# Performance work log

Measured on AMD Instinct MI355X. Metric: run time of the kernel, lower is better.

Reference implementation:

```python
import jax, jax.numpy as jnp
import numpy as np

G, N, K, F = 256, 512, 6, 64  # graphs, nodes/graph, knn k, n_features
T = G * N

def leaky(x):
    return jnp.where(x >= 0, x, 0.2 * x)

def prelu(x, a):
    return jnp.where(x >= 0, x, a * x)

def knn_idx(x):
    # per-graph kNN (k=6, self excluded); idx[i] = global indices of 6 nearest nbrs of i
    xg = x.reshape(G, N, F)
    sq = jnp.sum(xg * xg, axis=-1)                       # [G,N]
    d = sq[:, :, None] + sq[:, None, :] - 2.0 * jnp.einsum('gnf,gmf->gnm', xg, xg)
    d = jnp.where(jnp.eye(N, dtype=bool)[None], jnp.inf, d)  # loop=False
    _, idx = jax.lax.top_k(-d, K)                        # [G,N,K] local indices
    idx = idx + (jnp.arange(G) * N)[:, None, None]       # make global
    return idx.reshape(T, K)

def gconv(h, idx, W, b):
    # PyG GeneralConv defaults: out[i] = sum_{j in nbr(i)} (x_j W + b) + x_i
    s = jnp.take(h, idx, axis=0).sum(axis=1)             # [T,F] sum of neighbor feats
    return s @ W + K * b + h

def forward(x, W1, b1, a1, W2, b2, a2,
            Wc1, bc1, Wc2, bc2, Wc3, bc3, Wc4, bc4,
            W3, b3, a3, W4, b4, a4,
            Wh1, bh1, Wh2, bh2, Wh3, bh3, Wh4, bh4, idx):
    h = prelu(x @ W1 + b1, a1)
    h = prelu(h @ W2 + b2, a2)
    h = gconv(h, idx, Wc1, bc1)
    h = gconv(h, idx, Wc2, bc2)
    h = gconv(h, idx, Wc3, bc3)
    h = gconv(h, idx, Wc4, bc4)
    h = prelu(h @ W3 + b3, a3)
    h = prelu(h @ W4 + b4, a4)
    pooled = h.reshape(G, N, F).sum(axis=1)              # global_add_pool -> [G,F]
    y = leaky(pooled @ Wh1 + bh1)
    y = leaky(y @ Wh2 + bh2)
    y = leaky(y @ Wh3 + bh3)
    return y @ Wh4 + bh4                                 # [G,1]

def setup_inputs():
    key = jax.random.key(0)
    ks = jax.random.split(key, 16)
    def lin(k, i, o):
        k1, k2 = jax.random.split(k)
        s = 1.0 / np.sqrt(i)
        return (jax.random.uniform(k1, (i, o), jnp.float32, -s, s),
                jax.random.uniform(k2, (o,), jnp.float32, -s, s))
    inp = {"x": jax.random.normal(ks[0], (T, F), jnp.float32)}
    W1, b1 = lin(ks[1], F, F); W2, b2 = lin(ks[2], F, F)
    Wc1, bc1 = lin(ks[3], F, F); Wc2, bc2 = lin(ks[4], F, F)
    Wc3, bc3 = lin(ks[5], F, F); Wc4, bc4 = lin(ks[6], F, F)
    W3, b3 = lin(ks[7], F, F); W4, b4 = lin(ks[8], F, F)
    Wh1, bh1 = lin(ks[9], F, 4 * F); Wh2, bh2 = lin(ks[10], 4 * F, 4 * F)
    Wh3, bh3 = lin(ks[11], 4 * F, F); Wh4, bh4 = lin(ks[12], F, 1)
    a = 0.25 * jnp.ones((F,), jnp.float32)  # PReLU init
    inp.update(W1=W1, b1=b1, a1=a, W2=W2, b2=b2, a2=a,
               Wc1=Wc1, bc1=bc1, Wc2=Wc2, bc2=bc2, Wc3=Wc3, bc3=bc3, Wc4=Wc4, bc4=bc4,
               W3=W3, b3=b3, a3=a, W4=W4, b4=b4, a4=a,
               Wh1=Wh1, bh1=bh1, Wh2=Wh2, bh2=bh2, Wh3=Wh3, bh3=bh3, Wh4=Wh4, bh4=bh4)
    return inp

def reference(x, W1, b1, a1, W2, b2, a2, Wc1, bc1, Wc2, bc2, Wc3, bc3, Wc4, bc4,
              W3, b3, a3, W4, b4, a4, Wh1, bh1, Wh2, bh2, Wh3, bh3, Wh4, bh4):
    idx = knn_idx(x)  # edge_index built from raw x, as in the torch module
    return forward(x, W1, b1, a1, W2, b2, a2, Wc1, bc1, Wc2, bc2, Wc3, bc3, Wc4, bc4,
                   W3, b3, a3, W4, b4, a4, Wh1, bh1, Wh2, bh2, Wh3, bh3, Wh4, bh4, idx)
```

## Files before the change

kernel.cpp:

```cpp
#include <hip/hip_runtime.h>

#define NGRAPH 256
#define NNODE  512
#define KNN    6
#define NCAND  12
#define NF     64
#define SBF    72
#define NT     768
#define NW     12
#define PBF    18432
#define CANDO  PBF
#define SQO    (PBF + 3072)
#define WTO    36864
#define LDS_FLOATS 39168
#define LDS_BYTES  (LDS_FLOATS*4)
#define POOLP  PBF
#define POOLED (PBF + 1024)
#define Y1OFF  (PBF + 1088)
#define Y2OFF  (PBF + 1344)
#define Y3OFF  (PBF + 1600)
#define BIG 1e30f

typedef float v4f __attribute__((ext_vector_type(4)));
typedef float v2f __attribute__((ext_vector_type(2)));
typedef short v8s __attribute__((ext_vector_type(8)));

struct Params {
  const float *x;
  const float *W1,*b1,*a1, *W2,*b2,*a2;
  const float *Wc0,*bc0, *Wc1,*bc1, *Wc2,*bc2, *Wc3,*bc3;
  const float *W3,*b3,*a3, *W4,*b4,*a4;
  const float *Wh1,*bh1, *Wh2,*bh2, *Wh3,*bh3, *Wh4,*bh4;
  float *out;
};

__device__ __forceinline__ unsigned f2bf(float x) {
  union { float f; unsigned u; } cc; cc.f = x;
  unsigned u = cc.u;
  return (u + 0x7FFFu + ((u >> 16) & 1u)) >> 16;
}
__device__ __forceinline__ float bflo(unsigned u) {
  union { unsigned u; float f; } c; c.u = u << 16; return c.f;
}
__device__ __forceinline__ float bfhi(unsigned u) {
  union { unsigned u; float f; } c; c.u = u & 0xffff0000u; return c.f;
}
__device__ __forceinline__ v2f up2(unsigned u) {
  v2f r; r.x = bflo(u); r.y = bfhi(u); return r;
}

__device__ __forceinline__ v8s bfrag(const unsigned short* base, int row, int c0) {
  return *(const v8s*)(base + row*SBF + c0);
}

__device__ __forceinline__ float packe(float e, int j) {
  return __uint_as_float((__float_as_uint(e) & 0xFFFFFE00u) | (unsigned)j);
}

__device__ __forceinline__ void ins8(float (&b)[8], float v) {
  if (v < b[7]) {
#pragma unroll
    for (int p = 0; p < 8; ++p) {
      float lo = fminf(b[p], v);
      v = fmaxf(b[p], v);
      b[p] = lo;
    }
  }
}
__device__ __forceinline__ void ins12(float (&b)[NCAND], float v) {
  if (v < b[NCAND-1]) {
#pragma unroll
    for (int p = 0; p < NCAND; ++p) {
      float lo = fminf(b[p], v);
      v = fmaxf(b[p], v);
      b[p] = lo;
    }
  }
}

__device__ __forceinline__ void stage_wt(const float* W, unsigned short* wt, int tid) {
  const int col = tid >> 3, ks = (tid & 7) * 8;
  const float* wp = W + col;
  unsigned d[4];
#pragma unroll
  for (int i = 0; i < 4; ++i) {
    unsigned lo = f2bf(wp[(ks + 2*i    ) * NF]);
    unsigned hi = f2bf(wp[(ks + 2*i + 1) * NF]);
    d[i] = lo | (hi << 16);
  }
  *(uint4*)&wt[col*SBF + ks] = make_uint4(d[0], d[1], d[2], d[3]);
}

__global__ __launch_bounds__(NT) void fused_gnn(Params P) {
  extern __shared__ float lds[];
  unsigned short* hbf  = (unsigned short*)lds;
  unsigned short* pbf  = (unsigned short*)&lds[PBF];
  unsigned short* wt   = (unsigned short*)&lds[WTO];
  unsigned short* cand = (unsigned short*)&lds[CANDO];
  const int tid  = threadIdx.x;
  const int g    = blockIdx.x;
  const int rA   = tid;
  const int lane = tid & 63;
  const int w    = tid >> 6;
  const int c    = lane & 15;
  const int qq   = lane >> 4;

  const float* xgp = P.x + (size_t)g * NNODE * NF;
  const float4* xg = (const float4*)xgp;

#pragma unroll 1
  for (int i = tid; i < NNODE*NF/4; i += NT) {
    float4 v = xg[i];
    int row = i >> 4, k4 = i & 15;
    unsigned lo = f2bf(v.x) | (f2bf(v.y) << 16);
    unsigned hi = f2bf(v.z) | (f2bf(v.w) << 16);
    *(uint2*)&hbf[row*SBF + 4*k4] = make_uint2(lo, hi);
  }
  __syncthreads();

  if (tid < 512) {
    const uint4* xr = (const uint4*)(hbf + rA*SBF);
    float s = 0.f;
#pragma unroll
    for (int k = 0; k < 8; ++k) {
      uint4 u = xr[k];
      float f;
      f = bflo(u.x); s = fmaf(f, f, s); f = bfhi(u.x); s = fmaf(f, f, s);
      f = bflo(u.y); s = fmaf(f, f, s); f = bfhi(u.y); s = fmaf(f, f, s);
      f = bflo(u.z); s = fmaf(f, f, s); f = bfhi(u.z); s = fmaf(f, f, s);
      f = bflo(u.w); s = fmaf(f, f, s); f = bfhi(u.w); s = fmaf(f, f, s);
    }
    lds[SQO + rA] = s;
  }
  __syncthreads();

  {
#pragma unroll 1
    for (int tt = w; tt < 32; tt += NW) {
      const int i0 = tt * 16;
      v8s A0 = bfrag(hbf, i0 + c, qq*8);
      v8s A1 = bfrag(hbf, i0 + c, 32 + qq*8);
      const int myrow = i0 + c;

      float d8[8];
#pragma unroll
      for (int m = 0; m < 8; ++m) d8[m] = BIG;

#pragma unroll 2
      for (int jt = 0; jt < 32; ++jt) {
        const int j0 = jt * 16;
        v8s B0 = bfrag(hbf, j0 + c, qq*8);
        v8s B1 = bfrag(hbf, j0 + c, 32 + qq*8);
        v4f acc = {0.f, 0.f, 0.f, 0.f};
        acc = __builtin_amdgcn_mfma_f32_16x16x32_bf16(B0, A0, acc, 0, 0, 0);
        acc = __builtin_amdgcn_mfma_f32_16x16x32_bf16(B1, A1, acc, 0, 0, 0);
        float4 sv = *(const float4*)&lds[SQO + j0 + qq*4];
        float e0 = fmaf(-2.f, acc[0], sv.x);
        float e1 = fmaf(-2.f, acc[1], sv.y);
        float e2 = fmaf(-2.f, acc[2], sv.z);
        float e3 = fmaf(-2.f, acc[3], sv.w);
        const int jb = j0 + qq*4;
        if (jt == tt) {
          if (jb     == myrow) e0 = BIG;
          if (jb + 1 == myrow) e1 = BIG;
          if (jb + 2 == myrow) e2 = BIG;
          if (jb + 3 == myrow) e3 = BIG;
        }
        ins8(d8, packe(e0, jb));
        ins8(d8, packe(e1, jb+1));
        ins8(d8, packe(e2, jb+2));
        ins8(d8, packe(e3, jb+3));
      }

      float cd[NCAND];
#pragma unroll
      for (int m = 0; m < 8; ++m) cd[m] = d8[m];
#pragma unroll
      for (int m = 8; m < NCAND; ++m) cd[m] = BIG;
      {
        float pd[8];
#pragma unroll
        for (int s = 0; s < 8; ++s) pd[s] = __shfl_xor(cd[s], 16);
#pragma unroll
        for (int s = 0; s < 8; ++s) ins12(cd, pd[s]);
      }
      {
        float pd[NCAND];
#pragma unroll
        for (int s = 0; s < NCAND; ++s) pd[s] = __shfl_xor(cd[s], 32);
#pragma unroll
        for (int s = 0; s < NCAND; ++s) ins12(cd, pd[s]);
      }
      if (lane < 16) {
#pragma unroll
        for (int s = 0; s < NCAND; ++s)
          cand[(i0 + lane)*NCAND + s] =
            (unsigned short)(__float_as_uint(cd[s]) & 0x1FFu);
      }
    }
  }
  __syncthreads();

  if (tid < 512) {
    const float4* xrow = (const float4*)(xgp + rA*NF);
    float s0 = 0.f;
#pragma unroll
    for (int k4 = 0; k4 < 16; ++k4) {
      float4 a = xrow[k4];
      s0 = fmaf(a.x,a.x,s0); s0 = fmaf(a.y,a.y,s0); s0 = fmaf(a.z,a.z,s0); s0 = fmaf(a.w,a.w,s0);
    }
    lds[SQO + rA] = s0;
  }
  __syncthreads();

  int nbrA[KNN];
  if (tid < 512) {
    const float4* xrow = (const float4*)(xgp + rA*NF);
    float nd[6]; int ni[6];
#pragma unroll
    for (int m = 0; m < 6; ++m) { nd[m] = BIG; ni[m] = 0x7fffffff; }
    int cnd[NCAND];
#pragma unroll
    for (int s = 0; s < NCAND; ++s) cnd[s] = cand[rA*NCAND + s];

#pragma unroll 1
    for (int s = 0; s < NCAND; ++s) {
      int j = cnd[s];
      const float4* xj = (const float4*)(xgp + j*NF);
      float4 aa = {0.f, 0.f, 0.f, 0.f};
#pragma unroll
      for (int k4 = 0; k4 < 16; ++k4) {
        float4 a = xrow[k4];
        float4 v = xj[k4];
        aa.x = fmaf(a.x, v.x, aa.x); aa.y = fmaf(a.y, v.y, aa.y);
        aa.z = fmaf(a.z, v.z, aa.z); aa.w = fmaf(a.w, v.w, aa.w);
      }
      float e = fmaf(-2.f, (aa.x+aa.y)+(aa.z+aa.w), lds[SQO + j]);
      if (e < nd[5] || (e == nd[5] && j < ni[5])) {
#pragma unroll
        for (int pp = 0; pp < 6; ++pp) {
          bool lt = (e < nd[pp]) || (e == nd[pp] && j < ni[pp]);
          float tb2 = nd[pp]; int ti = ni[pp];
          nd[pp] = lt ? e : tb2;  ni[pp] = lt ? j : ti;
          e      = lt ? tb2 : e;  j      = lt ? ti : j;
        }
      }
    }
#pragma unroll
    for (int m = 0; m < 6; ++m) nbrA[m] = ni[m];
  }

#pragma unroll 1
  for (int L = 0; L < 8; ++L) {
    const bool isconv = (L >= 2 && L <= 5);
    const float* Wl = L==0?P.W1 : L==1?P.W2 : L==2?P.Wc0 : L==3?P.Wc1 :
                      L==4?P.Wc2 : L==5?P.Wc3 : L==6?P.W3 : P.W4;
    const float* bl = L==0?P.b1 : L==1?P.b2 : L==2?P.bc0 : L==3?P.bc1 :
                      L==4?P.bc2 : L==5?P.bc3 : L==6?P.b3 : P.b4;
    const float* al = L==0?P.a1 : L==1?P.a2 : L==6?P.a3 : P.a4;

    __syncthreads();
    if (tid < 512) stage_wt(Wl, wt, tid);
    __syncthreads();

    v8s B0[4], B1[4];
#pragma unroll
    for (int n = 0; n < 4; ++n) {
      B0[n] = bfrag(wt, n*16 + c, qq*8);
      B1[n] = bfrag(wt, n*16 + c, 32 + qq*8);
    }
    float br[4], ar[4];
    if (!isconv) {
#pragma unroll
      for (int n = 0; n < 4; ++n) { br[n] = bl[n*16 + c]; ar[n] = al[n*16 + c]; }
    }

#pragma unroll 1
    for (int tt = w; tt < 32; tt += NW) {
      const int i0 = tt * 16;
      v8s A0 = bfrag(hbf, i0 + c, qq*8);
      v8s A1 = bfrag(hbf, i0 + c, 32 + qq*8);
#pragma unroll
      for (int n = 0; n < 4; ++n) {
        v4f acc = {0.f, 0.f, 0.f, 0.f};
        acc = __builtin_amdgcn_mfma_f32_16x16x32_bf16(A0, B0[n], acc, 0, 0, 0);
        acc = __builtin_amdgcn_mfma_f32_16x16x32_bf16(A1, B1[n], acc, 0, 0, 0);
        if (isconv) {
#pragma unroll
          for (int r = 0; r < 4; ++r)
            pbf[(i0 + qq*4 + r)*SBF + n*16 + c] = (unsigned short)f2bf(acc[r]);
        } else {
#pragma unroll
          for (int r = 0; r < 4; ++r) {
            float v = acc[r] + br[n];
            v = v >= 0.f ? v : ar[n]*v;
            hbf[(i0 + qq*4 + r)*SBF + n*16 + c] = (unsigned short)f2bf(v);
          }
        }
      }
    }

    if (isconv) {
      __syncthreads();
      if (tid < 512) {
        const float4* bp = (const float4*)bl;
#pragma unroll 1
        for (int ch = 0; ch < 4; ++ch) {
          const int co = ch*16;
          v2f a2[8];
          {
            const uint4* hr = (const uint4*)&hbf[rA*SBF + co];
            uint4 u0 = hr[0], u1 = hr[1];
            a2[0]=up2(u0.x); a2[1]=up2(u0.y); a2[2]=up2(u0.z); a2[3]=up2(u0.w);
            a2[4]=up2(u1.x); a2[5]=up2(u1.y); a2[6]=up2(u1.z); a2[7]=up2(u1.w);
          }
          {
            float4 b0 = bp[ch*4+0], b1 = bp[ch*4+1], b2 = bp[ch*4+2], b3 = bp[ch*4+3];
            v2f t;
            t.x=b0.x; t.y=b0.y; a2[0] += 6.f*t;  t.x=b0.z; t.y=b0.w; a2[1] += 6.f*t;
            t.x=b1.x; t.y=b1.y; a2[2] += 6.f*t;  t.x=b1.z; t.y=b1.w; a2[3] += 6.f*t;
            t.x=b2.x; t.y=b2.y; a2[4] += 6.f*t;  t.x=b2.z; t.y=b2.w; a2[5] += 6.f*t;
            t.x=b3.x; t.y=b3.y; a2[6] += 6.f*t;  t.x=b3.z; t.y=b3.w; a2[7] += 6.f*t;
          }
#pragma unroll
          for (int mm = 0; mm < KNN; ++mm) {
            const uint4* pr = (const uint4*)&pbf[nbrA[mm]*SBF + co];
            uint4 p0 = pr[0], p1 = pr[1];
            a2[0]+=up2(p0.x); a2[1]+=up2(p0.y); a2[2]+=up2(p0.z); a2[3]+=up2(p0.w);
            a2[4]+=up2(p1.x); a2[5]+=up2(p1.y); a2[6]+=up2(p1.z); a2[7]+=up2(p1.w);
          }
          uint4 o0, o1;
          o0.x = f2bf(a2[0].x) | (f2bf(a2[0].y) << 16);
          o0.y = f2bf(a2[1].x) | (f2bf(a2[1].y) << 16);
          o0.z = f2bf(a2[2].x) | (f2bf(a2[2].y) << 16);
          o0.w = f2bf(a2[3].x) | (f2bf(a2[3].y) << 16);
          o1.x = f2bf(a2[4].x) | (f2bf(a2[4].y) << 16);
          o1.y = f2bf(a2[5].x) | (f2bf(a2[5].y) << 16);
          o1.z = f2bf(a2[6].x) | (f2bf(a2[6].y) << 16);
          o1.w = f2bf(a2[7].x) | (f2bf(a2[7].y) << 16);
          uint4* hw = (uint4*)&hbf[rA*SBF + co];
          hw[0] = o0; hw[1] = o1;
        }
      }
    }
  }
  __syncthreads();

  if (tid < 512) {
    int f2 = tid & 31, cch = tid >> 5;
    int rstart = cch * 32;
    const unsigned* h32 = (const unsigned*)hbf;
    v2f s2; s2.x = 0.f; s2.y = 0.f;
#pragma unroll 1
    for (int r = 0; r < 32; ++r) s2 += up2(h32[(rstart + r)*(SBF/2) + f2]);
    *(float2*)&lds[POOLP + cch*64 + 2*f2] = make_float2(s2.x, s2.y);
  }
  __syncthreads();
  if (tid < 64) {
    float pool = 0.f;
#pragma unroll
    for (int cc = 0; cc < 16; ++cc) pool += lds[POOLP + cc*64 + tid];
    lds[POOLED + tid] = pool;
  }
  __syncthreads();

  if (tid < 256) {
    float acc = P.bh1[tid];
#pragma unroll 4
    for (int k = 0; k < 64; ++k) acc = fmaf(lds[POOLED+k], P.Wh1[k*256 + tid], acc);
    lds[Y1OFF + tid] = acc >= 0.f ? acc : 0.2f*acc;
  }
  __syncthreads();
  if (tid < 512) {
    int o = tid & 255, hh = tid >> 8;
    float acc = hh ? 0.f : P.bh2[o];
    const int k0 = hh * 128;
#pragma unroll 4
    for (int k = k0; k < k0 + 128; ++k) acc = fmaf(lds[Y1OFF+k], P.Wh2[k*256 + o], acc);
    lds[POOLP + hh*256 + o] = acc;
  }
  __syncthreads();
  if (tid < 256) {
    float acc = lds[POOLP + tid] + lds[POOLP + 256 + tid];
    lds[Y2OFF + tid] = acc >= 0.f ? acc : 0.2f*acc;
  }
  __syncthreads();
  if (tid < 64) {
    float acc = P.bh3[tid];
#pragma unroll 4
    for (int k = 0; k < 256; ++k) acc = fmaf(lds[Y2OFF+k], P.Wh3[k*64 + tid], acc);
    lds[Y3OFF + tid] = acc >= 0.f ? acc : 0.2f*acc;
  }
  __syncthreads();
  if (tid == 0) {
    float acc = P.bh4[0];
#pragma unroll 4
    for (int k = 0; k < 64; ++k) acc = fmaf(lds[Y3OFF+k], P.Wh4[k], acc);
    P.out[g] = acc;
  }
}

extern "C" void kernel_launch(void* const* d_in, const int* in_sizes, int n_in,
                              void* d_out, int out_size, void* d_ws, size_t ws_size,
                              hipStream_t stream) {
  Params P;
  P.x   = (const float*)d_in[0];
  P.W1  = (const float*)d_in[1];  P.b1  = (const float*)d_in[2];  P.a1 = (const float*)d_in[3];
  P.W2  = (const float*)d_in[4];  P.b2  = (const float*)d_in[5];  P.a2 = (const float*)d_in[6];
  P.Wc0 = (const float*)d_in[7];  P.bc0 = (const float*)d_in[8];
  P.Wc1 = (const float*)d_in[9];  P.bc1 = (const float*)d_in[10];
  P.Wc2 = (const float*)d_in[11]; P.bc2 = (const float*)d_in[12];
  P.Wc3 = (const float*)d_in[13]; P.bc3 = (const float*)d_in[14];
  P.W3  = (const float*)d_in[15]; P.b3  = (const float*)d_in[16]; P.a3 = (const float*)d_in[17];
  P.W4  = (const float*)d_in[18]; P.b4  = (const float*)d_in[19]; P.a4 = (const float*)d_in[20];
  P.Wh1 = (const float*)d_in[21]; P.bh1 = (const float*)d_in[22];
  P.Wh2 = (const float*)d_in[23]; P.bh2 = (const float*)d_in[24];
  P.Wh3 = (const float*)d_in[25]; P.bh3 = (const float*)d_in[26];
  P.Wh4 = (const float*)d_in[27]; P.bh4 = (const float*)d_in[28];
  P.out = (float*)d_out;

  (void)hipFuncSetAttribute(reinterpret_cast<const void*>(fused_gnn),
                            hipFuncAttributeMaxDynamicSharedMemorySize, LDS_BYTES);

  fused_gnn<<<NGRAPH, NT, LDS_BYTES, stream>>>(P);
}
```

Before: 314.6 us.

## Rebalance kNN filter tiles per wave, spread gconv gather over all threads, parallelize head tail

The kNN MFMA filter previously gave 12 waves a strided set of the 32 row tiles, which left the work uneven. Now waves 0-7 take 3 tiles each and waves 8-11 take 2, and each wave shares every B-fragment load across its tiles. Neighbor indices move from per-thread registers to LDS, so the gconv aggregation can run on all 768 threads with 8 lanes per row covering 8 features each, instead of 512 threads looping over 4 chunks. The last two head layers are also split across 256 threads, with a wave shuffle reduction for the final dot product. The costs are more registers in the multi-tile filter and extra LDS space and traffic for the neighbor table.

```diff
diff --git a/kernel.cpp b/kernel.cpp
--- a/kernel.cpp
+++ b/kernel.cpp
@@ -12,13 +12,13 @@
 #define CANDO  PBF
 #define SQO    (PBF + 3072)
 #define WTO    36864
-#define LDS_FLOATS 39168
+#define NBRO   39168
+#define LDS_FLOATS 40704
 #define LDS_BYTES  (LDS_FLOATS*4)
 #define POOLP  PBF
 #define POOLED (PBF + 1024)
 #define Y1OFF  (PBF + 1088)
 #define Y2OFF  (PBF + 1344)
-#define Y3OFF  (PBF + 1600)
 #define BIG 1e30f
 
 typedef float v4f __attribute__((ext_vector_type(4)));
@@ -91,12 +91,89 @@
   *(uint4*)&wt[col*SBF + ks] = make_uint4(d[0], d[1], d[2], d[3]);
 }
 
+template<int NTILE>
+__device__ __forceinline__ void filter_tiles(const unsigned short* hbf,
+                                             const float* ldsf,
+                                             unsigned short* cand,
+                                             const int (&tts)[NTILE],
+                                             int lane, int c, int qq) {
+  v8s A0[NTILE], A1[NTILE];
+  float d8[NTILE][8];
+  int i0[NTILE];
+#pragma unroll
+  for (int k = 0; k < NTILE; ++k) {
+    i0[k] = tts[k] * 16;
+    A0[k] = bfrag(hbf, i0[k] + c, qq*8);
+    A1[k] = bfrag(hbf, i0[k] + c, 32 + qq*8);
+#pragma unroll
+    for (int m = 0; m < 8; ++m) d8[k][m] = BIG;
+  }
+#pragma unroll 1
+  for (int jt = 0; jt < 32; ++jt) {
+    const int j0 = jt * 16;
+    v8s B0 = bfrag(hbf, j0 + c, qq*8);
+    v8s B1 = bfrag(hbf, j0 + c, 32 + qq*8);
+    float4 sv = *(const float4*)&ldsf[SQO + j0 + qq*4];
+    const int jb = j0 + qq*4;
+#pragma unroll
+    for (int k = 0; k < NTILE; ++k) {
+      v4f acc = {0.f, 0.f, 0.f, 0.f};
+      acc = __builtin_amdgcn_mfma_f32_16x16x32_bf16(B0, A0[k], acc, 0, 0, 0);
+      acc = __builtin_amdgcn_mfma_f32_16x16x32_bf16(B1, A1[k], acc, 0, 0, 0);
+      float e0 = fmaf(-2.f, acc[0], sv.x);
+      float e1 = fmaf(-2.f, acc[1], sv.y);
+      float e2 = fmaf(-2.f, acc[2], sv.z);
+      float e3 = fmaf(-2.f, acc[3], sv.w);
+      if (jt == tts[k]) {
+        const int myrow = i0[k] + c;
+        if (jb     == myrow) e0 = BIG;
+        if (jb + 1 == myrow) e1 = BIG;
+        if (jb + 2 == myrow) e2 = BIG;
+        if (jb + 3 == myrow) e3 = BIG;
+      }
+      ins8(d8[k], packe(e0, jb));
+      ins8(d8[k], packe(e1, jb+1));
+      ins8(d8[k], packe(e2, jb+2));
+      ins8(d8[k], packe(e3, jb+3));
+    }
+  }
+#pragma unroll
+  for (int k = 0; k < NTILE; ++k) {
+    float cd[NCAND];
+#pragma unroll
+    for (int m = 0; m < 8; ++m) cd[m] = d8[k][m];
+#pragma unroll
+    for (int m = 8; m < NCAND; ++m) cd[m] = BIG;
+    {
+      float pd[8];
+#pragma unroll
+      for (int s = 0; s < 8; ++s) pd[s] = __shfl_xor(cd[s], 16);
+#pragma unroll
+      for (int s = 0; s < 8; ++s) ins12(cd, pd[s]);
+    }
+    {
+      float pd[NCAND];
+#pragma unroll
+      for (int s = 0; s < NCAND; ++s) pd[s] = __shfl_xor(cd[s], 32);
+#pragma unroll
+      for (int s = 0; s < NCAND; ++s) ins12(cd, pd[s]);
+    }
+    if (lane < 16) {
+#pragma unroll
+      for (int s = 0; s < NCAND; ++s)
+        cand[(i0[k] + lane)*NCAND + s] =
+          (unsigned short)(__float_as_uint(cd[s]) & 0x1FFu);
+    }
+  }
+}
+
 __global__ __launch_bounds__(NT) void fused_gnn(Params P) {
   extern __shared__ float lds[];
   unsigned short* hbf  = (unsigned short*)lds;
   unsigned short* pbf  = (unsigned short*)&lds[PBF];
   unsigned short* wt   = (unsigned short*)&lds[WTO];
   unsigned short* cand = (unsigned short*)&lds[CANDO];
+  unsigned short* nbrs = (unsigned short*)&lds[NBRO];
   const int tid  = threadIdx.x;
   const int g    = blockIdx.x;
   const int rA   = tid;
@@ -134,70 +211,12 @@
   }
   __syncthreads();
 
-  {
-#pragma unroll 1
-    for (int tt = w; tt < 32; tt += NW) {
-      const int i0 = tt * 16;
-      v8s A0 = bfrag(hbf, i0 + c, qq*8);
-      v8s A1 = bfrag(hbf, i0 + c, 32 + qq*8);
-      const int myrow = i0 + c;
-
-      float d8[8];
-#pragma unroll
-      for (int m = 0; m < 8; ++m) d8[m] = BIG;
-
-#pragma unroll 2
-      for (int jt = 0; jt < 32; ++jt) {
-        const int j0 = jt * 16;
-        v8s B0 = bfrag(hbf, j0 + c, qq*8);
-        v8s B1 = bfrag(hbf, j0 + c, 32 + qq*8);
-        v4f acc = {0.f, 0.f, 0.f, 0.f};
-        acc = __builtin_amdgcn_mfma_f32_16x16x32_bf16(B0, A0, acc, 0, 0, 0);
-        acc = __builtin_amdgcn_mfma_f32_16x16x32_bf16(B1, A1, acc, 0, 0, 0);
-        float4 sv = *(const float4*)&lds[SQO + j0 + qq*4];
-        float e0 = fmaf(-2.f, acc[0], sv.x);
-        float e1 = fmaf(-2.f, acc[1], sv.y);
-        float e2 = fmaf(-2.f, acc[2], sv.z);
-        float e3 = fmaf(-2.f, acc[3], sv.w);
-        const int jb = j0 + qq*4;
-        if (jt == tt) {
-          if (jb     == myrow) e0 = BIG;
-          if (jb + 1 == myrow) e1 = BIG;
-          if (jb + 2 == myrow) e2 = BIG;
-          if (jb + 3 == myrow) e3 = BIG;
-        }
-        ins8(d8, packe(e0, jb));
-        ins8(d8, packe(e1, jb+1));
-        ins8(d8, packe(e2, jb+2));
-        ins8(d8, packe(e3, jb+3));
-      }
-
-      float cd[NCAND];
-#pragma unroll
-      for (int m = 0; m < 8; ++m) cd[m] = d8[m];
-#pragma unroll
-      for (int m = 8; m < NCAND; ++m) cd[m] = BIG;
-      {
-        float pd[8];
-#pragma unroll
-        for (int s = 0; s < 8; ++s) pd[s] = __shfl_xor(cd[s], 16);
-#pragma unroll
-        for (int s = 0; s < 8; ++s) ins12(cd, pd[s]);
-      }
-      {
-        float pd[NCAND];
-#pragma unroll
-        for (int s = 0; s < NCAND; ++s) pd[s] = __shfl_xor(cd[s], 32);
-#pragma unroll
-        for (int s = 0; s < NCAND; ++s) ins12(cd, pd[s]);
-      }
-      if (lane < 16) {
-#pragma unroll
-        for (int s = 0; s < NCAND; ++s)
-          cand[(i0 + lane)*NCAND + s] =
-            (unsigned short)(__float_as_uint(cd[s]) & 0x1FFu);
-      }
-    }
+  if (w < 8) {
+    int tts[3] = {w, w + 8, w + 16};
+    filter_tiles<3>(hbf, lds, cand, tts, lane, c, qq);
+  } else {
+    int tts[2] = {w + 16, w + 20};
+    filter_tiles<2>(hbf, lds, cand, tts, lane, c, qq);
   }
   __syncthreads();
 
@@ -213,7 +232,6 @@
   }
   __syncthreads();
 
-  int nbrA[KNN];
   if (tid < 512) {
     const float4* xrow = (const float4*)(xgp + rA*NF);
     float nd[6]; int ni[6];
@@ -247,7 +265,7 @@
       }
     }
 #pragma unroll
-    for (int m = 0; m < 6; ++m) nbrA[m] = ni[m];
+    for (int m = 0; m < 6; ++m) nbrs[rA*KNN + m] = (unsigned short)ni[m];
   }
 
 #pragma unroll 1
@@ -302,44 +320,33 @@
 
     if (isconv) {
       __syncthreads();
-      if (tid < 512) {
-        const float4* bp = (const float4*)bl;
-#pragma unroll 1
-        for (int ch = 0; ch < 4; ++ch) {
-          const int co = ch*16;
-          v2f a2[8];
-          {
-            const uint4* hr = (const uint4*)&hbf[rA*SBF + co];
-            uint4 u0 = hr[0], u1 = hr[1];
-            a2[0]=up2(u0.x); a2[1]=up2(u0.y); a2[2]=up2(u0.z); a2[3]=up2(u0.w);
-            a2[4]=up2(u1.x); a2[5]=up2(u1.y); a2[6]=up2(u1.z); a2[7]=up2(u1.w);
+      {
+        const int s = tid & 7;
+        const float* bls = bl + 8*s;
+        float4 bv0 = *(const float4*)(bls);
+        float4 bv1 = *(const float4*)(bls + 4);
+#pragma unroll 1
+        for (int r = tid >> 3; r < NNODE; r += NT/8) {
+          const unsigned short* nb = &nbrs[r*KNN];
+          uint4 own = *(const uint4*)&hbf[r*SBF + 8*s];
+          v2f a0 = up2(own.x), a1 = up2(own.y), a2 = up2(own.z), a3 = up2(own.w);
+          v2f t;
+          t.x = bv0.x; t.y = bv0.y; a0 += 6.f*t;
+          t.x = bv0.z; t.y = bv0.w; a1 += 6.f*t;
+          t.x = bv1.x; t.y = bv1.y; a2 += 6.f*t;
+          t.x = bv1.z; t.y = bv1.w; a3 += 6.f*t;
+#pragma unroll
+          for (int mm = 0; mm < KNN; ++mm) {
+            int nbr = nb[mm];
+            uint4 p = *(const uint4*)&pbf[nbr*SBF + 8*s];
+            a0 += up2(p.x); a1 += up2(p.y); a2 += up2(p.z); a3 += up2(p.w);
           }
-          {
-            float4 b0 = bp[ch*4+0], b1 = bp[ch*4+1], b2 = bp[ch*4+2], b3 = bp[ch*4+3];
-            v2f t;
-            t.x=b0.x; t.y=b0.y; a2[0] += 6.f*t;  t.x=b0.z; t.y=b0.w; a2[1] += 6.f*t;
-            t.x=b1.x; t.y=b1.y; a2[2] += 6.f*t;  t.x=b1.z; t.y=b1.w; a2[3] += 6.f*t;
-            t.x=b2.x; t.y=b2.y; a2[4] += 6.f*t;  t.x=b2.z; t.y=b2.w; a2[5] += 6.f*t;
-            t.x=b3.x; t.y=b3.y; a2[6] += 6.f*t;  t.x=b3.z; t.y=b3.w; a2[7] += 6.f*t;
-          }
-#pragma unroll
-          for (int mm = 0; mm < KNN; ++mm) {
-            const uint4* pr = (const uint4*)&pbf[nbrA[mm]*SBF + co];
-            uint4 p0 = pr[0], p1 = pr[1];
-            a2[0]+=up2(p0.x); a2[1]+=up2(p0.y); a2[2]+=up2(p0.z); a2[3]+=up2(p0.w);
-            a2[4]+=up2(p1.x); a2[5]+=up2(p1.y); a2[6]+=up2(p1.z); a2[7]+=up2(p1.w);
-          }
-          uint4 o0, o1;
-          o0.x = f2bf(a2[0].x) | (f2bf(a2[0].y) << 16);
-          o0.y = f2bf(a2[1].x) | (f2bf(a2[1].y) << 16);
-          o0.z = f2bf(a2[2].x) | (f2bf(a2[2].y) << 16);
-          o0.w = f2bf(a2[3].x) | (f2bf(a2[3].y) << 16);
-          o1.x = f2bf(a2[4].x) | (f2bf(a2[4].y) << 16);
-          o1.y = f2bf(a2[5].x) | (f2bf(a2[5].y) << 16);
-          o1.z = f2bf(a2[6].x) | (f2bf(a2[6].y) << 16);
-          o1.w = f2bf(a2[7].x) | (f2bf(a2[7].y) << 16);
-          uint4* hw = (uint4*)&hbf[rA*SBF + co];
-          hw[0] = o0; hw[1] = o1;
+          uint4 o;
+          o.x = f2bf(a0.x) | (f2bf(a0.y) << 16);
+          o.y = f2bf(a1.x) | (f2bf(a1.y) << 16);
+          o.z = f2bf(a2.x) | (f2bf(a2.y) << 16);
+          o.w = f2bf(a3.x) | (f2bf(a3.y) << 16);
+          *(uint4*)&hbf[r*SBF + 8*s] = o;
         }
       }
     }
@@ -385,18 +392,23 @@
     lds[Y2OFF + tid] = acc >= 0.f ? acc : 0.2f*acc;
   }
   __syncthreads();
+  if (tid < 256) {
+    int o = tid & 63, hh = tid >> 6;
+    float acc = 0.f;
+    const int k0 = hh * 64;
+#pragma unroll 4
+    for (int k = k0; k < k0 + 64; ++k) acc = fmaf(lds[Y2OFF+k], P.Wh3[k*64 + o], acc);
+    lds[POOLP + hh*64 + o] = acc;
+  }
+  __syncthreads();
   if (tid < 64) {
-    float acc = P.bh3[tid];
-#pragma unroll 4
-    for (int k = 0; k < 256; ++k) acc = fmaf(lds[Y2OFF+k], P.Wh3[k*64 + tid], acc);
-    lds[Y3OFF + tid] = acc >= 0.f ? acc : 0.2f*acc;
-  }
-  __syncthreads();
-  if (tid == 0) {
-    float acc = P.bh4[0];
-#pragma unroll 4
-    for (int k = 0; k < 64; ++k) acc = fmaf(lds[Y3OFF+k], P.Wh4[k], acc);
-    P.out[g] = acc;
+    float acc = P.bh3[tid] + lds[POOLP + tid] + lds[POOLP + 64 + tid]
+              + lds[POOLP + 128 + tid] + lds[POOLP + 192 + tid];
+    float y3 = acc >= 0.f ? acc : 0.2f*acc;
+    float v = y3 * P.Wh4[tid];
+#pragma unroll
+    for (int off = 32; off >= 1; off >>= 1) v += __shfl_down(v, off);
+    if (tid == 0) P.out[g] = v + P.bh4[0];
   }
 }
 
```

New measurement: 308.7 us. Within noise of the previous version (-1.9%).
